# Optimization experiments

Hardware: AMD Instinct MI355X
Metric: run time of the kernel (lower is better)

The kernel has to match this reference:

```python
import jax, jax.numpy as jnp
import numpy as np
from math import sqrt

N_HEADS = 16

def setup_inputs() -> dict:
    key = jax.random.key(0)
    ks = jax.random.split(key, 6)
    B, T, C = 4, 2048, 1024
    s = 0.02
    return {
        "X": jax.random.normal(ks[0], (B, T, C), jnp.float32),
        "Wq": jax.random.normal(ks[1], (C, C), jnp.float32) * s,
        "Wk": jax.random.normal(ks[2], (C, C), jnp.float32) * s,
        "Wv": jax.random.normal(ks[3], (C, C), jnp.float32) * s,
        "Wo": jax.random.normal(ks[4], (C, C), jnp.float32) * s,
        "bo": jnp.zeros((C,), jnp.float32),
    }

def reference(X, Wq, Wk, Wv, Wo, bo):
    B, T, C = X.shape
    H = N_HEADS
    D = C // H
    scale = sqrt(C / H)  # == sqrt(D)
    # Linear layers (torch Linear: y = x @ W.T), split into heads: [B,H,T,D]
    Q = (X @ Wq.T).reshape(B, T, H, D).transpose(0, 2, 1, 3)
    K = (X @ Wk.T).reshape(B, T, H, D).transpose(0, 2, 1, 3)
    V = (X @ Wv.T).reshape(B, T, H, D).transpose(0, 2, 1, 3)
    A = jnp.einsum("bhtd,bhsd->bhts", Q, K) / scale  # [B,H,T,T]
    causal = jnp.tril(jnp.ones((T, T), dtype=bool))
    A = jnp.where(causal, A, -jnp.inf)
    A = jax.nn.softmax(A, axis=-1)
    Y = jnp.einsum("bhts,bhsd->bhtd", A, V)  # [B,H,T,D]
    Y = Y.transpose(0, 2, 1, 3).reshape(B, T, C)
    return Y @ Wo.T + bo
```

## Files before the change

### kernel.cpp

```cpp
#include <hip/hip_runtime.h>
#include <hip/hip_bf16.h>
#include <stdint.h>


typedef unsigned short u16;
typedef __attribute__((ext_vector_type(8))) __bf16 bf16x8;
typedef __attribute__((ext_vector_type(4))) float  f32x4;
typedef __attribute__((ext_vector_type(4))) unsigned short u16x4;
typedef __attribute__((ext_vector_type(8))) unsigned short u16x8;
typedef __attribute__((ext_vector_type(4))) short s16x4;

#define B_  4
#define T_  2048
#define C_  1024
#define H_  16
#define D_  64
#define BT_ (B_ * T_)

#define Q_SCALE 0.1803368801111204f

__device__ __forceinline__ u16 f32_to_bf16(float f) {
    unsigned int u = __float_as_uint(f);
    unsigned int r = (u + 0x7FFFu + ((u >> 16) & 1u)) >> 16;
    return (u16)r;
}

__device__ __forceinline__ unsigned int pk_bf16(float a, float b) {
    float2 f2; f2.x = a; f2.y = b;
    __hip_bfloat162 h = __float22bfloat162_rn(f2);
    return *(unsigned int*)&h;
}

__device__ __forceinline__ void async16(const void* g, void* lds) {
    __builtin_amdgcn_global_load_lds(
        (const __attribute__((address_space(1))) void*)g,
        (__attribute__((address_space(3))) void*)lds, 16, 0, 0);
}

__global__ void cast_bf16_kernel(const float* __restrict__ in, u16* __restrict__ out, int n4) {
    int i = blockIdx.x * 256 + threadIdx.x;
    if (i >= n4) return;
    float4 v = ((const float4*)in)[i];
    u16x4 o;
    o[0] = f32_to_bf16(v.x); o[1] = f32_to_bf16(v.y);
    o[2] = f32_to_bf16(v.z); o[3] = f32_to_bf16(v.w);
    ((u16x4*)out)[i] = o;
}

__global__ void cast_w4_kernel(const float* __restrict__ w0, const float* __restrict__ w1,
                               const float* __restrict__ w2, const float* __restrict__ w3,
                               u16* __restrict__ o0, u16* __restrict__ o1,
                               u16* __restrict__ o2, u16* __restrict__ o3) {
    int which = blockIdx.y;
    const float* in = (which == 0) ? w0 : (which == 1) ? w1 : (which == 2) ? w2 : w3;
    u16* out = (which == 0) ? o0 : (which == 1) ? o1 : (which == 2) ? o2 : o3;
    int i = blockIdx.x * 256 + threadIdx.x;
    float4 v = ((const float4*)in)[i];
    u16x4 o;
    o[0] = f32_to_bf16(v.x); o[1] = f32_to_bf16(v.y);
    o[2] = f32_to_bf16(v.z); o[3] = f32_to_bf16(v.w);
    ((u16x4*)out)[i] = o;
}

__global__ __launch_bounds__(256, 2) void qkv_gemm(
    const u16* __restrict__ Xb,
    const u16* __restrict__ Wqb, const u16* __restrict__ Wkb, const u16* __restrict__ Wvb,
    u16* __restrict__ Qb, u16* __restrict__ Kb, u16* __restrict__ Vtb)
{
    __shared__ u16 Xs[8192];
    __shared__ u16 Wqs[8192], Wks[8192], Wvs[8192];

    int id = blockIdx.x;
    int xcd = id & 7;
    int local = id >> 3;
    int tt = xcd * 8 + (local & 7);
    int ct = local >> 3;
    int m0 = tt * 128, n0 = ct * 128;

    int tid = threadIdx.x, lane = tid & 63, w = tid >> 6;
    int quad = lane >> 4, l15 = lane & 15;
    int wm = w >> 1, wn = w & 1;

    int c0 = tid, c1 = tid + 256;
    int row0 = c0 >> 2, row1 = c1 >> 2;
    int gc0 = (((c0 & 3) - (row0 >> 1)) & 3) * 8;
    int gc1 = (((c1 & 3) - (row1 >> 1)) & 3) * 8;
    int ldsb0 = (w * 64) * 16;
    int ldsb1 = (256 + w * 64) * 16;

    const u16* xp0 = Xb  + (size_t)(m0 + row0) * C_ + gc0;
    const u16* xp1 = Xb  + (size_t)(m0 + row1) * C_ + gc1;
    const u16* wq0 = Wqb + (size_t)(n0 + row0) * C_ + gc0;
    const u16* wq1 = Wqb + (size_t)(n0 + row1) * C_ + gc1;
    const u16* wk0 = Wkb + (size_t)(n0 + row0) * C_ + gc0;
    const u16* wk1 = Wkb + (size_t)(n0 + row1) * C_ + gc1;
    const u16* wv0 = Wvb + (size_t)(n0 + row0) * C_ + gc0;
    const u16* wv1 = Wvb + (size_t)(n0 + row1) * C_ + gc1;

    int aoff[4], boff[4];
#pragma unroll
    for (int i = 0; i < 4; ++i) {
        int rA = wm * 64 + i * 16 + l15;
        aoff[i] = (rA * 32 + (((rA >> 1) + quad) & 3) * 8) * 2;
        int rB = wn * 64 + i * 16 + l15;
        boff[i] = (rB * 32 + (((rB >> 1) + quad) & 3) * 8) * 2;
    }

    f32x4 aq[4][4], ak[4][4], av[4][4];
    const f32x4 z4 = {0.f, 0.f, 0.f, 0.f};
#pragma unroll
    for (int i = 0; i < 4; ++i)
#pragma unroll
        for (int j = 0; j < 4; ++j) { aq[i][j] = z4; ak[i][j] = z4; av[i][j] = z4; }

    async16(xp0, (char*)Xs  + ldsb0); async16(xp1, (char*)Xs  + ldsb1);
    async16(wq0, (char*)Wqs + ldsb0); async16(wq1, (char*)Wqs + ldsb1);
    async16(wk0, (char*)Wks + ldsb0); async16(wk1, (char*)Wks + ldsb1);
    async16(wv0, (char*)Wvs + ldsb0); async16(wv1, (char*)Wvs + ldsb1);
    xp0 += 32; xp1 += 32; wq0 += 32; wq1 += 32;
    wk0 += 32; wk1 += 32; wv0 += 32; wv1 += 32;

    auto body = [&](int kt, int cur, int nxt) {
        __syncthreads();
        if (kt + 1 < 32) {
            async16(xp0, (char*)Xs  + nxt + ldsb0); async16(xp1, (char*)Xs  + nxt + ldsb1);
            async16(wq0, (char*)Wqs + nxt + ldsb0); async16(wq1, (char*)Wqs + nxt + ldsb1);
            async16(wk0, (char*)Wks + nxt + ldsb0); async16(wk1, (char*)Wks + nxt + ldsb1);
            async16(wv0, (char*)Wvs + nxt + ldsb0); async16(wv1, (char*)Wvs + nxt + ldsb1);
        }
        xp0 += 32; xp1 += 32; wq0 += 32; wq1 += 32;
        wk0 += 32; wk1 += 32; wv0 += 32; wv1 += 32;

        bf16x8 xa[4];
#pragma unroll
        for (int i = 0; i < 4; ++i)
            xa[i] = *(const bf16x8*)((const char*)Xs + cur + aoff[i]);

        bf16x8 bb[4];
#pragma unroll
        for (int j = 0; j < 4; ++j)
            bb[j] = *(const bf16x8*)((const char*)Wqs + cur + boff[j]);
#pragma unroll
        for (int j = 0; j < 4; ++j)
#pragma unroll
            for (int i = 0; i < 4; ++i)
                aq[j][i] = __builtin_amdgcn_mfma_f32_16x16x32_bf16(bb[j], xa[i], aq[j][i], 0, 0, 0);

#pragma unroll
        for (int j = 0; j < 4; ++j)
            bb[j] = *(const bf16x8*)((const char*)Wks + cur + boff[j]);
#pragma unroll
        for (int j = 0; j < 4; ++j)
#pragma unroll
            for (int i = 0; i < 4; ++i)
                ak[j][i] = __builtin_amdgcn_mfma_f32_16x16x32_bf16(bb[j], xa[i], ak[j][i], 0, 0, 0);

#pragma unroll
        for (int j = 0; j < 4; ++j)
            bb[j] = *(const bf16x8*)((const char*)Wvs + cur + boff[j]);
#pragma unroll
        for (int i = 0; i < 4; ++i)
#pragma unroll
            for (int j = 0; j < 4; ++j)
                av[i][j] = __builtin_amdgcn_mfma_f32_16x16x32_bf16(xa[i], bb[j], av[i][j], 0, 0, 0);
    };

    for (int kt = 0; kt < 32; kt += 2) {
        body(kt,     0,    8192);
        body(kt + 1, 8192, 0);
    }

#pragma unroll
    for (int j = 0; j < 4; ++j) {
        int ch0 = n0 + wn * 64 + j * 16 + quad * 4;
#pragma unroll
        for (int i = 0; i < 4; ++i) {
            int t = m0 + wm * 64 + i * 16 + l15;
            u16x4 vq, vk;
#pragma unroll
            for (int r = 0; r < 4; ++r) {
                vq[r] = f32_to_bf16(aq[j][i][r] * Q_SCALE);
                vk[r] = f32_to_bf16(ak[j][i][r]);
            }
            *(u16x4*)&Qb[(size_t)t * C_ + ch0] = vq;
            *(u16x4*)&Kb[(size_t)t * C_ + ch0] = vk;
        }
    }
#pragma unroll
    for (int i = 0; i < 4; ++i) {
        int t0 = m0 + wm * 64 + i * 16 + quad * 4;
        int bb_ = t0 >> 11, tloc = t0 & (T_ - 1);
#pragma unroll
        for (int j = 0; j < 4; ++j) {
            int col = n0 + wn * 64 + j * 16 + l15;
            int h = col >> 6, d = col & 63;
            u16x4 v;
#pragma unroll
            for (int r = 0; r < 4; ++r) v[r] = f32_to_bf16(av[i][j][r]);
            *(u16x4*)&Vtb[(((bb_ * H_ + h) * D_ + d) * T_) + tloc] = v;
        }
    }
}

__device__ __forceinline__ void gemm_core_128_db(
    const u16* __restrict__ A, const u16* __restrict__ B,
    u16* As, u16* Bs, int m0, int n0, f32x4 (&acc)[4][4])
{
    const int K = C_;
    const int KT = K / 32;
    int tid  = threadIdx.x;
    int lane = tid & 63, w = tid >> 6;
    int quad = lane >> 4, l15 = lane & 15;
    int wm = w >> 1, wn = w & 1;

    int c0 = tid, c1 = tid + 256;
    int row0 = c0 >> 2, row1 = c1 >> 2;
    int gc0 = (((c0 & 3) - (row0 >> 1)) & 3) * 8;
    int gc1 = (((c1 & 3) - (row1 >> 1)) & 3) * 8;
    int ldsb0 = (w * 64) * 16;
    int ldsb1 = (256 + w * 64) * 16;

    const u16* ApA = A + (size_t)(m0 + row0) * K + gc0;
    const u16* ApB = A + (size_t)(m0 + row1) * K + gc1;
    const u16* BpA = B + (size_t)(n0 + row0) * K + gc0;
    const u16* BpB = B + (size_t)(n0 + row1) * K + gc1;

    char* As0 = (char*)As; char* As1 = (char*)As + 8192;
    char* Bs0 = (char*)Bs; char* Bs1 = (char*)Bs + 8192;

    int aoff[4], boff[4];
#pragma unroll
    for (int i = 0; i < 4; ++i) {
        int rA = wm * 64 + i * 16 + l15;
        aoff[i] = (rA * 32 + (((rA >> 1) + quad) & 3) * 8) * 2;
        int rB = wn * 64 + i * 16 + l15;
        boff[i] = (rB * 32 + (((rB >> 1) + quad) & 3) * 8) * 2;
    }

    async16(ApA, As0 + ldsb0); async16(ApB, As0 + ldsb1);
    async16(BpA, Bs0 + ldsb0); async16(BpB, Bs0 + ldsb1);
    ApA += 32; ApB += 32; BpA += 32; BpB += 32;

    auto body = [&](int kt, const char* Ac, const char* Bc, char* Apf, char* Bpf) {
        __syncthreads();
        if (kt + 1 < KT) {
            async16(ApA, Apf + ldsb0); async16(ApB, Apf + ldsb1);
            async16(BpA, Bpf + ldsb0); async16(BpB, Bpf + ldsb1);
        }
        ApA += 32; ApB += 32; BpA += 32; BpB += 32;

        bf16x8 a[4], b[4];
#pragma unroll
        for (int i = 0; i < 4; ++i) {
            a[i] = *(const bf16x8*)(Ac + aoff[i]);
            b[i] = *(const bf16x8*)(Bc + boff[i]);
        }
#pragma unroll
        for (int i = 0; i < 4; ++i)
#pragma unroll
            for (int j = 0; j < 4; ++j)
                acc[i][j] = __builtin_amdgcn_mfma_f32_16x16x32_bf16(a[i], b[j], acc[i][j], 0, 0, 0);
    };

    for (int kt = 0; kt < KT; kt += 2) {
        body(kt,     As0, Bs0, As1, Bs1);
        body(kt + 1, As1, Bs1, As0, Bs0);
    }
}

__global__ __launch_bounds__(256) void attn_kernel(
    const u16* __restrict__ Qb, const u16* __restrict__ Kb,
    const u16* __restrict__ Vtb, u16* __restrict__ Yb)
{
    __shared__ u16 SMA[16384];
    u16* Ks0 = SMA;
    u16* Ks1 = SMA + 4096;
    u16* Vs0 = SMA + 8192;
    u16* Vs1 = SMA + 12288;

    int id = blockIdx.x;
    int bh = id & 63;
    int jj = id >> 6;

    int tid = threadIdx.x, lane = tid & 63, w = tid >> 6;
    int quad = lane >> 4, l15 = lane & 15;
    int b = bh >> 4, h = bh & 15;

    int koff0[4], koff1[4], voff[4][4];
#pragma unroll
    for (int sblk = 0; sblk < 4; ++sblk) {
        int sr = sblk * 16 + l15;
        koff0[sblk] = (sr * 64 + ((quad + sr) & 7) * 8) * 2;
        koff1[sblk] = (sr * 64 + ((4 + quad + sr) & 7) * 8) * 2;
    }
#pragma unroll
    for (int n = 0; n < 4; ++n)
#pragma unroll
        for (int sblk = 0; sblk < 4; ++sblk) {
            int dr = n * 16 + l15;
            voff[n][sblk] = (dr * 64 + ((sblk * 2 + (quad >> 1) + dr) & 7) * 8 + (quad & 1) * 4) * 2;
        }

    int cA = tid, cB = tid + 256;
    int sA = cA >> 3, sB = cB >> 3;
    int offA = (((cA & 7) - sA) & 7) * 8;
    int offB = (((cB & 7) - sB) & 7) * 8;
    const u16* Kbase = Kb + (size_t)(b * T_) * C_ + h * 64;
    const u16* Vbase = Vtb + (size_t)bh * D_ * T_;
    int ldsb0 = (w * 64) * 16, ldsb1 = (256 + w * 64) * 16;

    const s16x4 ones = { (short)0x3F80, (short)0x3F80, (short)0x3F80, (short)0x3F80 };
    const f32x4 z4 = {0.f, 0.f, 0.f, 0.f};

    int qts[2] = { jj, 15 - jj };

    for (int pass = 0; pass < 2; ++pass) {
        int qt = qts[pass];
        int qbase = qt * 128;

        if (pass) __syncthreads();

        bf16x8 qf[2][2];
        {
            const u16* q0 = Qb + ((size_t)(b * T_ + qbase + w * 32 + l15)) * C_ + h * 64;
            qf[0][0] = *(const bf16x8*)(q0 + quad * 8);
            qf[0][1] = *(const bf16x8*)(q0 + 32 + quad * 8);
            const u16* q1 = q0 + 16 * C_;
            qf[1][0] = *(const bf16x8*)(q1 + quad * 8);
            qf[1][1] = *(const bf16x8*)(q1 + 32 + quad * 8);
        }

        f32x4 o_acc[2][4];
        f32x4 l_acc[2];
#pragma unroll
        for (int c = 0; c < 2; ++c) {
            l_acc[c] = z4;
#pragma unroll
            for (int n = 0; n < 4; ++n) o_acc[c][n] = z4;
        }

        const int nst = 2 * qt + 2;

        const u16* kgpA = Kbase + (size_t)sA * C_ + offA;
        const u16* kgpB = Kbase + (size_t)sB * C_ + offB;
        const u16* vgpA = Vbase + sA * T_ + offA;
        const u16* vgpB = Vbase + sB * T_ + offB;

        async16(kgpA, (char*)Ks0 + ldsb0);
        async16(kgpB, (char*)Ks0 + ldsb1);
        async16(vgpA, (char*)Vs0 + ldsb0);
        async16(vgpB, (char*)Vs0 + ldsb1);
        kgpA += 64 * C_; kgpB += 64 * C_; vgpA += 64; vgpB += 64;

        auto tile_body = [&](int st, const u16* K_, const u16* V_, char* Kpf, char* Vpf) {
            __syncthreads();
            if (st + 1 < nst) {
                async16(kgpA, Kpf + ldsb0);
                async16(kgpB, Kpf + ldsb1);
                async16(vgpA, Vpf + ldsb0);
                async16(vgpB, Vpf + ldsb1);
            }
            kgpA += 64 * C_; kgpB += 64 * C_; vgpA += 64; vgpB += 64;

            f32x4 sv[2][4];
#pragma unroll
            for (int sblk = 0; sblk < 4; ++sblk) {
                bf16x8 k0 = *(const bf16x8*)((const char*)K_ + koff0[sblk]);
                bf16x8 k1 = *(const bf16x8*)((const char*)K_ + koff1[sblk]);
#pragma unroll
                for (int c = 0; c < 2; ++c) {
                    f32x4 t0 = __builtin_amdgcn_mfma_f32_16x16x32_bf16(k0, qf[c][0], z4, 0, 0, 0);
                    sv[c][sblk] = __builtin_amdgcn_mfma_f32_16x16x32_bf16(k1, qf[c][1], t0, 0, 0, 0);
                }
            }

            if (st >= 2 * qt) {
                int sb0 = st * 64 - qbase;
#pragma unroll
                for (int c = 0; c < 2; ++c) {
                    int tl = w * 32 + c * 16 + l15;
#pragma unroll
                    for (int sblk = 0; sblk < 4; ++sblk)
#pragma unroll
                        for (int r = 0; r < 4; ++r)
                            if (sb0 + sblk * 16 + quad * 4 + r > tl) sv[c][sblk][r] = -1e30f;
                }
            }

            s16x4 pfrag[2][4];
#pragma unroll
            for (int c = 0; c < 2; ++c) {
#pragma unroll
                for (int sblk = 0; sblk < 4; ++sblk) {
#pragma unroll
                    for (int r = 0; r < 4; ++r)
                        sv[c][sblk][r] = __builtin_amdgcn_exp2f(sv[c][sblk][r]);
                    uint2 pk;
                    pk.x = pk_bf16(sv[c][sblk][0], sv[c][sblk][1]);
                    pk.y = pk_bf16(sv[c][sblk][2], sv[c][sblk][3]);
                    pfrag[c][sblk] = *(s16x4*)&pk;
                    l_acc[c] = __builtin_amdgcn_mfma_f32_16x16x16bf16_1k(ones, pfrag[c][sblk], l_acc[c], 0, 0, 0);
                }
            }

#pragma unroll
            for (int n = 0; n < 4; ++n)
#pragma unroll
                for (int sblk = 0; sblk < 4; ++sblk) {
                    s16x4 va = *(const s16x4*)((const char*)V_ + voff[n][sblk]);
#pragma unroll
                    for (int c = 0; c < 2; ++c)
                        o_acc[c][n] = __builtin_amdgcn_mfma_f32_16x16x16bf16_1k(va, pfrag[c][sblk], o_acc[c][n], 0, 0, 0);
                }
        };

        for (int st = 0; st < nst; st += 2) {
            tile_body(st,     Ks0, Vs0, (char*)Ks1, (char*)Vs1);
            tile_body(st + 1, Ks1, Vs1, (char*)Ks0, (char*)Vs0);
        }

        __syncthreads();
        u16* PW = SMA + w * 2304;
#pragma unroll
        for (int c = 0; c < 2; ++c) {
            float inv = 1.0f / l_acc[c][0];
#pragma unroll
            for (int n = 0; n < 4; ++n) {
                u16x4 v;
                uint2 pk;
                pk.x = pk_bf16(o_acc[c][n][0] * inv, o_acc[c][n][1] * inv);
                pk.y = pk_bf16(o_acc[c][n][2] * inv, o_acc[c][n][3] * inv);
                v = *(u16x4*)&pk;
                *(u16x4*)&PW[(c * 16 + l15) * 72 + n * 16 + quad * 4] = v;
            }
        }
        asm volatile("s_waitcnt lgkmcnt(0)" ::: "memory");
#pragma unroll
        for (int st = 0; st < 4; ++st) {
            int tr = st * 8 + (lane >> 3);
            int d8 = (lane & 7) * 8;
            u16x8 v = *(u16x8*)&PW[tr * 72 + d8];
            *(u16x8*)&Yb[(size_t)(b * T_ + qbase + w * 32 + tr) * C_ + h * 64 + d8] = v;
        }
    }
}

__global__ __launch_bounds__(256, 4) void proj_gemm(
    const u16* __restrict__ Yb, const u16* __restrict__ Wob,
    const float* __restrict__ bo, float* __restrict__ out)
{
    __shared__ u16 SM[17408];
    u16* As = SM;
    u16* Bs = SM + 8192;

    int id = blockIdx.x;
    int xcd = id & 7;
    int local = id >> 3;
    int by = xcd * 8 + (local & 7);
    int bx = local >> 3;
    int m0 = bx * 128, n0 = by * 128;

    f32x4 acc[4][4];
    const f32x4 z4 = {0.f, 0.f, 0.f, 0.f};
#pragma unroll
    for (int i = 0; i < 4; ++i)
#pragma unroll
        for (int j = 0; j < 4; ++j) acc[i][j] = z4;

    gemm_core_128_db(Wob, Yb, As, Bs, m0, n0, acc);

    int lane = threadIdx.x & 63, w = threadIdx.x >> 6;
    int quad = lane >> 4, l15 = lane & 15;
    int wm = w >> 1, wn = w & 1;

    float* LF = (float*)SM;
    __syncthreads();
#pragma unroll
    for (int hh = 0; hh < 2; ++hh) {
        if (wm == hh) {
#pragma unroll
            for (int i = 0; i < 4; ++i) {
                int chl = i * 16 + quad * 4;
#pragma unroll
                for (int j = 0; j < 4; ++j) {
                    int tl = wn * 64 + j * 16 + l15;
                    *(f32x4*)&LF[tl * 68 + chl] = acc[i][j];
                }
            }
        }
        __syncthreads();
        f32x4 b4 = *(const f32x4*)&bo[m0 + hh * 64 + (lane & 15) * 4];
#pragma unroll
        for (int st = 0; st < 8; ++st) {
            int tl = w * 32 + st * 4 + (lane >> 4);
            int ch4 = (lane & 15) * 4;
            f32x4 v = *(f32x4*)&LF[tl * 68 + ch4];
            v += b4;
            *(f32x4*)&out[(size_t)(n0 + tl) * C_ + m0 + hh * 64 + ch4] = v;
        }
        if (hh == 0) __syncthreads();
    }
}

extern "C" void kernel_launch(void* const* d_in, const int* in_sizes, int n_in,
                              void* d_out, int out_size, void* d_ws, size_t ws_size,
                              hipStream_t stream) {
    const float* X  = (const float*)d_in[0];
    const float* Wq = (const float*)d_in[1];
    const float* Wk = (const float*)d_in[2];
    const float* Wv = (const float*)d_in[3];
    const float* Wo = (const float*)d_in[4];
    const float* bo = (const float*)d_in[5];

    char* ws = (char*)d_ws;
    u16* Xb  = (u16*)(ws);
    u16* Wqb = (u16*)(ws + (16u << 20));
    u16* Wkb = (u16*)(ws + (18u << 20));
    u16* Wvb = (u16*)(ws + (20u << 20));
    u16* Wob = (u16*)(ws + (22u << 20));
    u16* Qb  = (u16*)(ws + (24u << 20));
    u16* Kb  = (u16*)(ws + (40u << 20));
    u16* Vtb = (u16*)(ws + (56u << 20));
    u16* Yb  = (u16*)(ws + (72u << 20));

    cast_bf16_kernel<<<(BT_ * C_ / 4) / 256, 256, 0, stream>>>(X, Xb, BT_ * C_ / 4);
    cast_w4_kernel<<<dim3((C_ * C_ / 4) / 256, 4), 256, 0, stream>>>(
        Wq, Wk, Wv, Wo, Wqb, Wkb, Wvb, Wob);

    qkv_gemm<<<dim3(512), 256, 0, stream>>>(Xb, Wqb, Wkb, Wvb, Qb, Kb, Vtb);
    attn_kernel<<<dim3(512), 256, 0, stream>>>(Qb, Kb, Vtb, Yb);
    proj_gemm<<<dim3(8 * 64), 256, 0, stream>>>(Yb, Wob, bo, (float*)d_out);
}
```

Measured before the change: 262.8 us.

## Halve attention query tile to 64 rows, double grid, merge cast kernels

The attention kernel now handles 64 query rows per block (16 per wave) instead of 128. It pairs tiles jj and 31-jj for causal load balance and launches 1024 blocks, with launch bounds allowing 4 blocks per CU to raise occupancy. The odd tile count is handled by a conditional second tile body. Separately, the X and weight cast kernels are merged into one launch to save a kernel launch. The trade-off is that each K/V tile loaded into LDS is now reused across half as many query rows, which doubles K/V traffic.

```diff
diff --git a/kernel.cpp b/kernel.cpp
--- a/kernel.cpp
+++ b/kernel.cpp
@@ -37,24 +37,22 @@
         (__attribute__((address_space(3))) void*)lds, 16, 0, 0);
 }
 
-__global__ void cast_bf16_kernel(const float* __restrict__ in, u16* __restrict__ out, int n4) {
-    int i = blockIdx.x * 256 + threadIdx.x;
-    if (i >= n4) return;
-    float4 v = ((const float4*)in)[i];
-    u16x4 o;
-    o[0] = f32_to_bf16(v.x); o[1] = f32_to_bf16(v.y);
-    o[2] = f32_to_bf16(v.z); o[3] = f32_to_bf16(v.w);
-    ((u16x4*)out)[i] = o;
-}
-
-__global__ void cast_w4_kernel(const float* __restrict__ w0, const float* __restrict__ w1,
-                               const float* __restrict__ w2, const float* __restrict__ w3,
-                               u16* __restrict__ o0, u16* __restrict__ o1,
-                               u16* __restrict__ o2, u16* __restrict__ o3) {
-    int which = blockIdx.y;
-    const float* in = (which == 0) ? w0 : (which == 1) ? w1 : (which == 2) ? w2 : w3;
-    u16* out = (which == 0) ? o0 : (which == 1) ? o1 : (which == 2) ? o2 : o3;
-    int i = blockIdx.x * 256 + threadIdx.x;
+__global__ void cast_all_kernel(const float* __restrict__ X,
+                                const float* __restrict__ w0, const float* __restrict__ w1,
+                                const float* __restrict__ w2, const float* __restrict__ w3,
+                                u16* __restrict__ xo,
+                                u16* __restrict__ o0, u16* __restrict__ o1,
+                                u16* __restrict__ o2, u16* __restrict__ o3) {
+    int id = blockIdx.x;
+    const float* in; u16* out; int i;
+    if (id < 8192) {
+        in = X; out = xo; i = id * 256 + threadIdx.x;
+    } else {
+        int k = (id - 8192) >> 10;
+        in  = (k == 0) ? w0 : (k == 1) ? w1 : (k == 2) ? w2 : w3;
+        out = (k == 0) ? o0 : (k == 1) ? o1 : (k == 2) ? o2 : o3;
+        i = ((id - 8192) & 1023) * 256 + threadIdx.x;
+    }
     float4 v = ((const float4*)in)[i];
     u16x4 o;
     o[0] = f32_to_bf16(v.x); o[1] = f32_to_bf16(v.y);
@@ -268,7 +266,7 @@
     }
 }
 
-__global__ __launch_bounds__(256) void attn_kernel(
+__global__ __launch_bounds__(256, 4) void attn_kernel(
     const u16* __restrict__ Qb, const u16* __restrict__ Kb,
     const u16* __restrict__ Vtb, u16* __restrict__ Yb)
 {
@@ -312,34 +310,27 @@
     const s16x4 ones = { (short)0x3F80, (short)0x3F80, (short)0x3F80, (short)0x3F80 };
     const f32x4 z4 = {0.f, 0.f, 0.f, 0.f};
 
-    int qts[2] = { jj, 15 - jj };
+    int qts[2] = { jj, 31 - jj };
 
     for (int pass = 0; pass < 2; ++pass) {
         int qt = qts[pass];
-        int qbase = qt * 128;
+        int qbase = qt * 64;
 
         if (pass) __syncthreads();
 
-        bf16x8 qf[2][2];
+        bf16x8 qf0, qf1;
         {
-            const u16* q0 = Qb + ((size_t)(b * T_ + qbase + w * 32 + l15)) * C_ + h * 64;
-            qf[0][0] = *(const bf16x8*)(q0 + quad * 8);
-            qf[0][1] = *(const bf16x8*)(q0 + 32 + quad * 8);
-            const u16* q1 = q0 + 16 * C_;
-            qf[1][0] = *(const bf16x8*)(q1 + quad * 8);
-            qf[1][1] = *(const bf16x8*)(q1 + 32 + quad * 8);
-        }
-
-        f32x4 o_acc[2][4];
-        f32x4 l_acc[2];
-#pragma unroll
-        for (int c = 0; c < 2; ++c) {
-            l_acc[c] = z4;
-#pragma unroll
-            for (int n = 0; n < 4; ++n) o_acc[c][n] = z4;
-        }
-
-        const int nst = 2 * qt + 2;
+            const u16* q0 = Qb + ((size_t)(b * T_ + qbase + w * 16 + l15)) * C_ + h * 64;
+            qf0 = *(const bf16x8*)(q0 + quad * 8);
+            qf1 = *(const bf16x8*)(q0 + 32 + quad * 8);
+        }
+
+        f32x4 o_acc[4];
+        f32x4 l_acc = z4;
+#pragma unroll
+        for (int n = 0; n < 4; ++n) o_acc[n] = z4;
+
+        const int nst = qt + 1;
 
         const u16* kgpA = Kbase + (size_t)sA * C_ + offA;
         const u16* kgpB = Kbase + (size_t)sB * C_ + offB;
@@ -362,45 +353,35 @@
             }
             kgpA += 64 * C_; kgpB += 64 * C_; vgpA += 64; vgpB += 64;
 
-            f32x4 sv[2][4];
+            f32x4 sv[4];
 #pragma unroll
             for (int sblk = 0; sblk < 4; ++sblk) {
                 bf16x8 k0 = *(const bf16x8*)((const char*)K_ + koff0[sblk]);
                 bf16x8 k1 = *(const bf16x8*)((const char*)K_ + koff1[sblk]);
-#pragma unroll
-                for (int c = 0; c < 2; ++c) {
-                    f32x4 t0 = __builtin_amdgcn_mfma_f32_16x16x32_bf16(k0, qf[c][0], z4, 0, 0, 0);
-                    sv[c][sblk] = __builtin_amdgcn_mfma_f32_16x16x32_bf16(k1, qf[c][1], t0, 0, 0, 0);
-                }
-            }
-
-            if (st >= 2 * qt) {
-                int sb0 = st * 64 - qbase;
-#pragma unroll
-                for (int c = 0; c < 2; ++c) {
-                    int tl = w * 32 + c * 16 + l15;
-#pragma unroll
-                    for (int sblk = 0; sblk < 4; ++sblk)
-#pragma unroll
-                        for (int r = 0; r < 4; ++r)
-                            if (sb0 + sblk * 16 + quad * 4 + r > tl) sv[c][sblk][r] = -1e30f;
-                }
-            }
-
-            s16x4 pfrag[2][4];
-#pragma unroll
-            for (int c = 0; c < 2; ++c) {
-#pragma unroll
-                for (int sblk = 0; sblk < 4; ++sblk) {
+                f32x4 t0 = __builtin_amdgcn_mfma_f32_16x16x32_bf16(k0, qf0, z4, 0, 0, 0);
+                sv[sblk] = __builtin_amdgcn_mfma_f32_16x16x32_bf16(k1, qf1, t0, 0, 0, 0);
+            }
+
+            if (st == qt) {
+                int tl = w * 16 + l15;
+#pragma unroll
+                for (int sblk = 0; sblk < 4; ++sblk)
 #pragma unroll
                     for (int r = 0; r < 4; ++r)
-                        sv[c][sblk][r] = __builtin_amdgcn_exp2f(sv[c][sblk][r]);
-                    uint2 pk;
-                    pk.x = pk_bf16(sv[c][sblk][0], sv[c][sblk][1]);
-                    pk.y = pk_bf16(sv[c][sblk][2], sv[c][sblk][3]);
-                    pfrag[c][sblk] = *(s16x4*)&pk;
-                    l_acc[c] = __builtin_amdgcn_mfma_f32_16x16x16bf16_1k(ones, pfrag[c][sblk], l_acc[c], 0, 0, 0);
-                }
+                        if (sblk * 16 + quad * 4 + r > tl) sv[sblk][r] = -1e30f;
+            }
+
+            s16x4 pfrag[4];
+#pragma unroll
+            for (int sblk = 0; sblk < 4; ++sblk) {
+#pragma unroll
+                for (int r = 0; r < 4; ++r)
+                    sv[sblk][r] = __builtin_amdgcn_exp2f(sv[sblk][r]);
+                uint2 pk;
+                pk.x = pk_bf16(sv[sblk][0], sv[sblk][1]);
+                pk.y = pk_bf16(sv[sblk][2], sv[sblk][3]);
+                pfrag[sblk] = *(s16x4*)&pk;
+                l_acc = __builtin_amdgcn_mfma_f32_16x16x16bf16_1k(ones, pfrag[sblk], l_acc, 0, 0, 0);
             }
 
 #pragma unroll
@@ -408,39 +389,35 @@
 #pragma unroll
                 for (int sblk = 0; sblk < 4; ++sblk) {
                     s16x4 va = *(const s16x4*)((const char*)V_ + voff[n][sblk]);
-#pragma unroll
-                    for (int c = 0; c < 2; ++c)
-                        o_acc[c][n] = __builtin_amdgcn_mfma_f32_16x16x16bf16_1k(va, pfrag[c][sblk], o_acc[c][n], 0, 0, 0);
+                    o_acc[n] = __builtin_amdgcn_mfma_f32_16x16x16bf16_1k(va, pfrag[sblk], o_acc[n], 0, 0, 0);
                 }
         };
 
         for (int st = 0; st < nst; st += 2) {
-            tile_body(st,     Ks0, Vs0, (char*)Ks1, (char*)Vs1);
-            tile_body(st + 1, Ks1, Vs1, (char*)Ks0, (char*)Vs0);
+            tile_body(st, Ks0, Vs0, (char*)Ks1, (char*)Vs1);
+            if (st + 1 < nst)
+                tile_body(st + 1, Ks1, Vs1, (char*)Ks0, (char*)Vs0);
         }
 
         __syncthreads();
-        u16* PW = SMA + w * 2304;
-#pragma unroll
-        for (int c = 0; c < 2; ++c) {
-            float inv = 1.0f / l_acc[c][0];
+        u16* PW = SMA + w * 1152;
+        {
+            float inv = 1.0f / l_acc[0];
 #pragma unroll
             for (int n = 0; n < 4; ++n) {
-                u16x4 v;
                 uint2 pk;
-                pk.x = pk_bf16(o_acc[c][n][0] * inv, o_acc[c][n][1] * inv);
-                pk.y = pk_bf16(o_acc[c][n][2] * inv, o_acc[c][n][3] * inv);
-                v = *(u16x4*)&pk;
-                *(u16x4*)&PW[(c * 16 + l15) * 72 + n * 16 + quad * 4] = v;
+                pk.x = pk_bf16(o_acc[n][0] * inv, o_acc[n][1] * inv);
+                pk.y = pk_bf16(o_acc[n][2] * inv, o_acc[n][3] * inv);
+                *(u16x4*)&PW[l15 * 72 + n * 16 + quad * 4] = *(u16x4*)&pk;
             }
         }
         asm volatile("s_waitcnt lgkmcnt(0)" ::: "memory");
 #pragma unroll
-        for (int st = 0; st < 4; ++st) {
+        for (int st = 0; st < 2; ++st) {
             int tr = st * 8 + (lane >> 3);
             int d8 = (lane & 7) * 8;
             u16x8 v = *(u16x8*)&PW[tr * 72 + d8];
-            *(u16x8*)&Yb[(size_t)(b * T_ + qbase + w * 32 + tr) * C_ + h * 64 + d8] = v;
+            *(u16x8*)&Yb[(size_t)(b * T_ + qbase + w * 16 + tr) * C_ + h * 64 + d8] = v;
         }
     }
 }
@@ -523,11 +500,10 @@
     u16* Vtb = (u16*)(ws + (56u << 20));
     u16* Yb  = (u16*)(ws + (72u << 20));
 
-    cast_bf16_kernel<<<(BT_ * C_ / 4) / 256, 256, 0, stream>>>(X, Xb, BT_ * C_ / 4);
-    cast_w4_kernel<<<dim3((C_ * C_ / 4) / 256, 4), 256, 0, stream>>>(
-        Wq, Wk, Wv, Wo, Wqb, Wkb, Wvb, Wob);
+    cast_all_kernel<<<dim3(8192 + 4 * 1024), 256, 0, stream>>>(
+        X, Wq, Wk, Wv, Wo, Xb, Wqb, Wkb, Wvb, Wob);
 
     qkv_gemm<<<dim3(512), 256, 0, stream>>>(Xb, Wqb, Wkb, Wvb, Qb, Kb, Vtb);
-    attn_kernel<<<dim3(512), 256, 0, stream>>>(Qb, Kb, Vtb, Yb);
+    attn_kernel<<<dim3(1024), 256, 0, stream>>>(Qb, Kb, Vtb, Yb);
     proj_gemm<<<dim3(8 * 64), 256, 0, stream>>>(Yb, Wob, bo, (float*)d_out);
 }
```

Measured after the change: 258.2 us. No clear change (-1.7%).
